# Performance work log

Measured on AMD Instinct MI355X. Metric: run time of the kernel, lower is better.

The kernel has to match this reference:

```python
import jax, jax.numpy as jnp
import numpy as np

EPS = 1e-5

def binary_activation(x):
    # ReActNet piecewise-polynomial STE: forward = sign(x), grad follows poly
    m1 = (x < -1).astype(x.dtype)
    m2 = (x < 0).astype(x.dtype)
    m3 = (x < 1).astype(x.dtype)
    out1 = -1.0 * m1 + (x * x + 2.0 * x) * (1.0 - m1)
    out2 = out1 * m2 + (-x * x + 2.0 * x) * (1.0 - m2)
    out3 = out2 * m3 + 1.0 * (1.0 - m3)
    return jax.lax.stop_gradient(jnp.sign(x) - out3) + out3

def binary_conv(x, w, stride, padding):
    # per-output-channel scaled sign weights with clamp STE
    scale = jnp.mean(jnp.abs(w), axis=(1, 2, 3), keepdims=True)
    clipped = jnp.clip(w, -1.0, 1.0)
    bw = jax.lax.stop_gradient(scale * jnp.sign(w) - clipped) + clipped
    return jax.lax.conv_general_dilated(
        x, bw, window_strides=(stride, stride),
        padding=[(padding, padding), (padding, padding)],
        dimension_numbers=('NCHW', 'OIHW', 'NCHW'))

def batch_norm(x, g, b):
    mu = jnp.mean(x, axis=(0, 2, 3), keepdims=True)
    var = jnp.mean((x - mu) ** 2, axis=(0, 2, 3), keepdims=True)
    xn = (x - mu) * jax.lax.rsqrt(var + EPS)
    return xn * g[None, :, None, None] + b[None, :, None, None]

def prelu(x, a):
    a = a[None, :, None, None]
    return jnp.where(x >= 0, x, a * x)

def setup_inputs() -> dict:
    key = jax.random.key(0)
    ks = jax.random.split(key, 12)
    N, C, H, W = 32, 256, 56, 56
    d = {
        'x': jax.random.normal(ks[0], (N, C, H, W), jnp.float32),
        'b11': jax.random.normal(ks[1], (1, C, 1, 1), jnp.float32) * 0.1,
        'b12': jax.random.normal(ks[2], (1, C, 1, 1), jnp.float32) * 0.1,
        'b13': jax.random.normal(ks[3], (1, C, 1, 1), jnp.float32) * 0.1,
        'b21': jax.random.normal(ks[4], (1, C, 1, 1), jnp.float32) * 0.1,
        'b22': jax.random.normal(ks[5], (1, C, 1, 1), jnp.float32) * 0.1,
        'b23': jax.random.normal(ks[6], (1, C, 1, 1), jnp.float32) * 0.1,
        'w3x3': jax.random.normal(ks[7], (C, C, 3, 3), jnp.float32) * 0.05,
        'wpw': jax.random.normal(ks[8], (C, C, 1, 1), jnp.float32) * 0.05,
        'g1': jnp.ones((C,), jnp.float32),
        'be1': jnp.zeros((C,), jnp.float32),
        'g2': jnp.ones((C,), jnp.float32),
        'be2': jnp.zeros((C,), jnp.float32),
        'p1': jnp.full((C,), 0.25, jnp.float32),
        'p2': jnp.full((C,), 0.25, jnp.float32),
    }
    return d

def reference(x, b11, b12, b13, b21, b22, b23, w3x3, wpw, g1, be1, g2, be2, p1, p2):
    # stride=1, inplanes == planes branch
    out1 = binary_activation(x + b11)
    out1 = binary_conv(out1, w3x3, stride=1, padding=1)
    out1 = batch_norm(out1, g1, be1)
    out1 = x + out1
    out1 = prelu(out1 + b12, p1) + b13
    out2 = binary_activation(out1 + b21)
    out2 = binary_conv(out2, wpw, stride=1, padding=0)
    out2 = batch_norm(out2, g2, be2)
    out2 = out2 + out1
    out2 = prelu(out2 + b22, p2) + b23
    return out2
```

## Files before the change

kernel.cpp:

```cpp
#include <hip/hip_runtime.h>

typedef __attribute__((ext_vector_type(4))) float  f32x4;
typedef __attribute__((ext_vector_type(4))) short  s16x4;
typedef __attribute__((ext_vector_type(4))) int    i32x4;

#define MFMAI8(a, b, c) __builtin_amdgcn_mfma_i32_16x16x64_i8((a), (b), (c), 0, 0, 0)

__device__ __forceinline__ void gload_lds16(const void* g, void* l) {
  __builtin_amdgcn_global_load_lds((const __attribute__((address_space(1))) void*)g,
                                   (__attribute__((address_space(3))) void*)l, 16, 0, 0);
}

__device__ __forceinline__ char sgn8(float v) {
  return v > 0.f ? (char)1 : (v < 0.f ? (char)-1 : (char)0);
}

__global__ __launch_bounds__(256) void prep_w(const float* __restrict__ w3,
                                              const float* __restrict__ wpw,
                                              char* __restrict__ w1s,
                                              char* __restrict__ w2s,
                                              float* __restrict__ scale1,
                                              float* __restrict__ scale2) {
  const int o = blockIdx.x;
  const int t = threadIdx.x;
  float s = 0.f;
  if (blockIdx.y == 0) {
    for (int u = t; u < 2304; u += 256) {
      int i = u / 9, tap = u % 9;
      float v = w3[(size_t)(o * 256 + i) * 9 + tap];
      s += fabsf(v);
      w1s[(size_t)(tap * 256 + o) * 256 + i] = sgn8(v);
    }
  } else {
    float v = wpw[o * 256 + t];
    s = fabsf(v);
    w2s[o * 256 + t] = sgn8(v);
  }
  for (int m = 1; m < 64; m <<= 1) s += __shfl_xor(s, m);
  __shared__ float red[4];
  if ((t & 63) == 0) red[t >> 6] = s;
  __syncthreads();
  if (t == 0) {
    float tot = red[0] + red[1] + red[2] + red[3];
    if (blockIdx.y == 0) scale1[o] = tot / 2304.f;
    else                 scale2[o] = tot / 256.f;
  }
}

__global__ __launch_bounds__(256) void sign_nhwc(const float* __restrict__ x,
                                                 const float* __restrict__ b11,
                                                 char* __restrict__ out) {
  __shared__ unsigned short l[56 * 128];
  __shared__ float cB[256];
  const int h = blockIdx.x, n = blockIdx.y, t = threadIdx.x;
  cB[t] = b11[t];
  __syncthreads();
  const int wv = t & 15, cg = t >> 4;
  if (wv < 14) {
    const int w0 = wv * 4;
    const int swz = (wv & 7) << 3;
#pragma unroll 4
    for (int it = 0; it < 8; ++it) {
      int cp = it * 16 + cg;
      int c0 = cp * 2;
      size_t i0 = (size_t)(n * 256 + c0) * 3136 + h * 56 + w0;
      f32x4 x0 = *(const f32x4*)(x + i0);
      f32x4 x1 = *(const f32x4*)(x + i0 + 3136);
      float bb0 = cB[c0], bb1 = cB[c0 + 1];
      int cs = cp ^ swz;
#pragma unroll
      for (int j = 0; j < 4; ++j) {
        unsigned short pk = (unsigned char)sgn8(x0[j] + bb0) |
                            ((unsigned short)(unsigned char)sgn8(x1[j] + bb1) << 8);
        l[(w0 + j) * 128 + cs] = pk;
      }
    }
  }
  __syncthreads();
  char* op = out + ((size_t)(n * 56 + h) * 56) * 256;
  for (int u = t; u < 56 * 16; u += 256) {
    int w2 = u >> 4, cp = u & 15;
    *(i32x4*)(op + w2 * 256 + cp * 16) =
        *(const i32x4*)&l[w2 * 128 + ((cp * 8) ^ (((w2 >> 2) & 7) << 3))];
  }
}

__global__ __launch_bounds__(256, 2) void conv3x3(const char* __restrict__ sIn,
                                                  const char* __restrict__ wSgn,
                                                  short* __restrict__ raw,
                                                  long long* __restrict__ S,
                                                  long long* __restrict__ SS) {
  __shared__ char lin[2][10 * 58 * 64];

  int bid = (blockIdx.x & 7) * 112 + (blockIdx.x >> 3);
  const int ot = bid & 3;
  const int g  = bid >> 2;
  const int ht = g % 7, n = g / 7;
  const int h0 = ht * 8, oc0 = ot * 64;

  const int t = threadIdx.x;
  const int lane = t & 63, wv = t >> 6;
  const int cl = lane & 15, kk = lane >> 4;

  if (t < 160) {
    int bi = t / 80, r = t % 80;
    int rr = r >> 3, q = r & 7;
    int col = (q >> 2) ? 57 : 0;
    *(i32x4*)&lin[bi][(rr * 58 + col) * 64 + (q & 3) * 16] = (i32x4){0, 0, 0, 0};
  }
  __syncthreads();

  const int pw = t >> 2, sl = t & 3;
  const int srcslot = sl ^ (((1 + pw) >> 1) & 3);

#define STAGE_3x3(icc, bi)                                                          \
  {                                                                                 \
    if (t < 224) {                                                                  \
      _Pragma("unroll")                                                             \
      for (int rr = 0; rr < 10; ++rr) {                                             \
        int h = h0 - 1 + rr;                                                        \
        char* dst = &lin[bi][(rr * 58 + 1 + pw) * 64 + sl * 16];                    \
        if (h >= 0 && h < 56) {                                                     \
          const char* src = sIn +                                                   \
              ((size_t)((n * 56 + h) * 56 + pw) * 256 + (icc) * 64 + srcslot * 16); \
          gload_lds16(src, dst);                                                    \
        } else {                                                                    \
          *(i32x4*)dst = (i32x4){0, 0, 0, 0};                                       \
        }                                                                           \
      }                                                                             \
    }                                                                               \
  }

  const char* wbase = wSgn + ((size_t)(oc0 + cl) << 8) + kk * 16;
#define WLOAD(dst, tap, icc)                                                        \
  {                                                                                 \
    _Pragma("unroll")                                                               \
    for (int m_ = 0; m_ < 4; ++m_)                                                  \
      dst[m_] = *(const i32x4*)(wbase + (size_t)(tap) * 65536 + m_ * 4096 + (icc) * 64); \
  }

  int r0[7], c0[7];
#pragma unroll
  for (int nf = 0; nf < 7; ++nf) {
    int p = wv * 112 + nf * 16 + cl;
    r0[nf] = p / 56;
    c0[nf] = p % 56;
  }

  i32x4 acc[4][7];
#pragma unroll
  for (int m = 0; m < 4; ++m)
#pragma unroll
    for (int nf = 0; nf < 7; ++nf) acc[m][nf] = (i32x4){0, 0, 0, 0};

  STAGE_3x3(0, 0);
  __syncthreads();

  i32x4 wA[4], wB[4];
  for (int icc = 0; icc < 4; ++icc) {
    const int cur = icc & 1;
    WLOAD(wA, 0, icc);
    WLOAD(wB, 1, icc);
    if (icc < 3) STAGE_3x3(icc + 1, cur ^ 1);

#pragma unroll
    for (int tap = 0; tap < 9; ++tap) {
      i32x4 w0 = wA[0], w1 = wA[1], w2 = wA[2], w3 = wA[3];
      wA[0] = wB[0]; wA[1] = wB[1]; wA[2] = wB[2]; wA[3] = wB[3];
      if (tap < 7) WLOAD(wB, tap + 2, icc);
      const int kh = tap / 3, kw = tap % 3;
#pragma unroll
      for (int nf = 0; nf < 7; ++nf) {
        int col = c0[nf] + kw;
        int addr = ((r0[nf] + kh) * 58 + col) * 64 + ((kk ^ ((col >> 1) & 3)) << 4);
        i32x4 b = *(const i32x4*)(&lin[cur][addr]);
        acc[0][nf] = MFMAI8(w0, b, acc[0][nf]);
        acc[1][nf] = MFMAI8(w1, b, acc[1][nf]);
        acc[2][nf] = MFMAI8(w2, b, acc[2][nf]);
        acc[3][nf] = MFMAI8(w3, b, acc[3][nf]);
      }
    }
    __syncthreads();
  }

  unsigned short* tb = (unsigned short*)&lin[0][0];
  const size_t ocbase = (size_t)n * 256 + oc0;
#pragma unroll
  for (int m = 0; m < 4; ++m) {
    int sm[4] = {0, 0, 0, 0};
    unsigned sq[4] = {0, 0, 0, 0};
#pragma unroll
    for (int nf = 0; nf < 7; ++nf) {
      i32x4 v = acc[m][nf];
#pragma unroll
      for (int r2 = 0; r2 < 4; ++r2) {
        sm[r2] += v[r2];
        sq[r2] += (unsigned)(v[r2] * v[r2]);
      }
    }
#pragma unroll
    for (int r2 = 0; r2 < 4; ++r2) {
      int aa = sm[r2];
      unsigned qq = sq[r2];
      aa += __shfl_xor(aa, 1); qq += __shfl_xor(qq, 1);
      aa += __shfl_xor(aa, 2); qq += __shfl_xor(qq, 2);
      aa += __shfl_xor(aa, 4); qq += __shfl_xor(qq, 4);
      aa += __shfl_xor(aa, 8); qq += __shfl_xor(qq, 8);
      if (cl == 0) {
        int oc = oc0 + m * 16 + kk * 4 + r2;
        atomicAdd((unsigned long long*)&S[oc], (unsigned long long)(long long)aa);
        atomicAdd((unsigned long long*)&SS[oc], (unsigned long long)qq);
      }
    }
    __syncthreads();
#pragma unroll
    for (int nf = 0; nf < 7; ++nf) {
      i32x4 v = acc[m][nf];
      int px = wv * 112 + nf * 16 + cl;
#pragma unroll
      for (int r2 = 0; r2 < 4; ++r2)
        tb[(kk * 4 + r2) * 472 + px] = (unsigned short)(short)v[r2];
    }
    __syncthreads();
    for (int u = t; u < 896; u += 256) {
      int qc = u >> 6, r = u & 63, ocl = r >> 2, c3 = r & 3;
      int c8 = qc * 4 + c3;
      *(i32x4*)(raw + (ocbase + m * 16 + ocl) * 3136 + h0 * 56 + c8 * 8) =
          *(const i32x4*)&tb[ocl * 472 + c8 * 8];
    }
  }
}

__global__ __launch_bounds__(256, 2) void conv1x1(const char* __restrict__ sIn,
                                                  const char* __restrict__ wSgn,
                                                  short* __restrict__ raw,
                                                  long long* __restrict__ S,
                                                  long long* __restrict__ SS) {
  __shared__ char lin[112 * 256];

  const int b = blockIdx.x;
  const int n = b / 28;
  const int hw0 = (b % 28) * 112;
  const size_t px0 = (size_t)n * 3136 + hw0;
  const int t = threadIdx.x, lane = t & 63, wv = t >> 6;
  const int cl = lane & 15, kk = lane >> 4;

#pragma unroll
  for (int i = 0; i < 7; ++i) {
    int u = i * 256 + t;
    int px = u >> 4, s = u & 15;
    const char* src = sIn + (px0 + px) * 256 + ((s ^ (px & 7)) * 16);
    gload_lds16(src, lin + u * 16);
  }

  i32x4 acc[4][7];
#pragma unroll
  for (int m = 0; m < 4; ++m)
#pragma unroll
    for (int nf = 0; nf < 7; ++nf) acc[m][nf] = (i32x4){0, 0, 0, 0};

  __syncthreads();

#pragma unroll
  for (int icc = 0; icc < 4; ++icc) {
    i32x4 bfr[7];
#pragma unroll
    for (int nf = 0; nf < 7; ++nf) {
      int px = nf * 16 + cl;
      int srd = (icc * 4 + kk) ^ (px & 7);
      bfr[nf] = *(const i32x4*)(lin + px * 256 + srd * 16);
    }
#pragma unroll
    for (int m = 0; m < 4; ++m) {
      i32x4 a = *(const i32x4*)(wSgn +
          (((size_t)(wv * 64 + m * 16 + cl)) << 8) + icc * 64 + kk * 16);
#pragma unroll
      for (int nf = 0; nf < 7; ++nf) acc[m][nf] = MFMAI8(a, bfr[nf], acc[m][nf]);
    }
  }

  __syncthreads();
  unsigned short* tb = (unsigned short*)lin;
#pragma unroll
  for (int m = 0; m < 4; ++m) {
    int sm[4] = {0, 0, 0, 0};
    unsigned sq[4] = {0, 0, 0, 0};
#pragma unroll
    for (int nf = 0; nf < 7; ++nf) {
      i32x4 v = acc[m][nf];
#pragma unroll
      for (int r2 = 0; r2 < 4; ++r2) {
        sm[r2] += v[r2];
        sq[r2] += (unsigned)(v[r2] * v[r2]);
      }
    }
#pragma unroll
    for (int r2 = 0; r2 < 4; ++r2) {
      int aa = sm[r2];
      unsigned qq = sq[r2];
      aa += __shfl_xor(aa, 1); qq += __shfl_xor(qq, 1);
      aa += __shfl_xor(aa, 2); qq += __shfl_xor(qq, 2);
      aa += __shfl_xor(aa, 4); qq += __shfl_xor(qq, 4);
      aa += __shfl_xor(aa, 8); qq += __shfl_xor(qq, 8);
      if (cl == 0) {
        int oc = wv * 64 + m * 16 + kk * 4 + r2;
        atomicAdd((unsigned long long*)&S[oc], (unsigned long long)(long long)aa);
        atomicAdd((unsigned long long*)&SS[oc], (unsigned long long)qq);
      }
    }
    __syncthreads();
#pragma unroll
    for (int nf = 0; nf < 7; ++nf) {
      i32x4 v = acc[m][nf];
      int px = nf * 16 + cl;
#pragma unroll
      for (int r2 = 0; r2 < 4; ++r2)
        tb[(wv * 16 + kk * 4 + r2) * 120 + px] = (unsigned short)(short)v[r2];
    }
    __syncthreads();
#pragma unroll
    for (int i = 0; i < 4; ++i) {
      int u = i * 256 + t;
      int ocg = u >> 4, c8 = u & 15;
      if (c8 < 14) {
        int oc = (ocg >> 4) * 64 + m * 16 + (ocg & 15);
        *(i32x4*)(raw + ((size_t)n * 256 + oc) * 3136 + hw0 + c8 * 8) =
            *(const i32x4*)&tb[ocg * 120 + c8 * 8];
      }
    }
  }
}

__global__ void bn_coef(const long long* __restrict__ S, const long long* __restrict__ SS,
                        const float* __restrict__ scale, const float* __restrict__ g,
                        const float* __restrict__ be, const float* __restrict__ bext,
                        float* __restrict__ A, float* __restrict__ B) {
  int o = threadIdx.x;
  const double invN = 1.0 / 100352.0;
  double mu_r  = (double)S[o] * invN;
  double var_r = (double)SS[o] * invN - mu_r * mu_r;
  double sc    = (double)scale[o];
  double rstd  = 1.0 / sqrt(sc * sc * var_r + 1e-5);
  double a     = (double)g[o] * rstd * sc;
  A[o] = (float)a;
  B[o] = (float)((double)be[o] - a * mu_r + (double)bext[o]);
}

__global__ __launch_bounds__(256) void mid_fuse(const short* __restrict__ raw,
                                                const float* __restrict__ x,
                                                const float* __restrict__ A1,
                                                const float* __restrict__ B1,
                                                const float* __restrict__ p1,
                                                const float* __restrict__ b13,
                                                const float* __restrict__ b21,
                                                float* __restrict__ t1,
                                                char* __restrict__ s2) {
  __shared__ unsigned short l[56 * 128];
  __shared__ float cA[256], cB[256], cP[256], cD[256], cE[256];
  const int h = blockIdx.x, n = blockIdx.y, t = threadIdx.x;
  cA[t] = A1[t]; cB[t] = B1[t]; cP[t] = p1[t]; cD[t] = b13[t]; cE[t] = b21[t];
  __syncthreads();
  const int wv = t & 15, cg = t >> 4;
  if (wv < 14) {
    const int w0 = wv * 4;
    const int swz = (wv & 7) << 3;
#pragma unroll 2
    for (int it = 0; it < 8; ++it) {
      int cp = it * 16 + cg;
      int c0 = cp * 2;
      size_t i0 = (size_t)(n * 256 + c0) * 3136 + h * 56 + w0;
      f32x4 x0 = *(const f32x4*)(x + i0);
      f32x4 x1 = *(const f32x4*)(x + i0 + 3136);
      s16x4 r0 = *(const s16x4*)(raw + i0);
      s16x4 r1 = *(const s16x4*)(raw + i0 + 3136);
      float a0 = cA[c0], b0 = cB[c0], p0 = cP[c0], d0 = cD[c0], e0 = cE[c0];
      float a1 = cA[c0+1], b1 = cB[c0+1], p1v = cP[c0+1], d1 = cD[c0+1], e1 = cE[c0+1];
      f32x4 o0, o1;
      int cs = cp ^ swz;
#pragma unroll
      for (int j = 0; j < 4; ++j) {
        float u0 = x0[j] + a0 * (float)r0[j] + b0;
        u0 = (u0 >= 0.f ? u0 : p0 * u0) + d0;
        o0[j] = u0;
        float u1 = x1[j] + a1 * (float)r1[j] + b1;
        u1 = (u1 >= 0.f ? u1 : p1v * u1) + d1;
        o1[j] = u1;
        unsigned short pk = (unsigned char)sgn8(u0 + e0) |
                            ((unsigned short)(unsigned char)sgn8(u1 + e1) << 8);
        l[(w0 + j) * 128 + cs] = pk;
      }
      *(f32x4*)(t1 + i0) = o0;
      *(f32x4*)(t1 + i0 + 3136) = o1;
    }
  }
  __syncthreads();
  char* op = s2 + ((size_t)(n * 56 + h) * 56) * 256;
  for (int u = t; u < 56 * 16; u += 256) {
    int w2 = u >> 4, cp = u & 15;
    *(i32x4*)(op + w2 * 256 + cp * 16) =
        *(const i32x4*)&l[w2 * 128 + ((cp * 8) ^ (((w2 >> 2) & 7) << 3))];
  }
}

__global__ __launch_bounds__(256) void final_fuse(const short* __restrict__ raw,
                                                  const float* __restrict__ A2,
                                                  const float* __restrict__ B2,
                                                  const float* __restrict__ p2,
                                                  const float* __restrict__ b23,
                                                  float* out) {
  const int c = blockIdx.x & 255;
  const size_t base = (size_t)blockIdx.x * 3136;
  const float a = A2[c], b = B2[c], p = p2[c], d = b23[c];
  for (int i = threadIdx.x; i < 784; i += 256) {
    s16x4 r  = *(const s16x4*)(raw + base + (size_t)i * 4);
    f32x4 tt = *(const f32x4*)(out + base + (size_t)i * 4);
    f32x4 o;
#pragma unroll
    for (int j = 0; j < 4; ++j) {
      float v = a * (float)r[j] + b + tt[j];
      o[j] = (v >= 0.f ? v : p * v) + d;
    }
    *(f32x4*)(out + base + (size_t)i * 4) = o;
  }
}

extern "C" void kernel_launch(void* const* d_in, const int* in_sizes, int n_in,
                              void* d_out, int out_size, void* d_ws, size_t ws_size,
                              hipStream_t stream) {
  const float* x   = (const float*)d_in[0];
  const float* b11 = (const float*)d_in[1];
  const float* b12 = (const float*)d_in[2];
  const float* b13 = (const float*)d_in[3];
  const float* b21 = (const float*)d_in[4];
  const float* b22 = (const float*)d_in[5];
  const float* b23 = (const float*)d_in[6];
  const float* w3  = (const float*)d_in[7];
  const float* wpw = (const float*)d_in[8];
  const float* g1  = (const float*)d_in[9];
  const float* be1 = (const float*)d_in[10];
  const float* g2  = (const float*)d_in[11];
  const float* be2 = (const float*)d_in[12];
  const float* p1  = (const float*)d_in[13];
  const float* p2  = (const float*)d_in[14];

  char* ws = (char*)d_ws;
  short*      raw    = (short*)(ws);
  char*       sgn    = (char*)(ws + 51380224);
  char*       w1s    = (char*)(ws + 77070336);
  char*       w2s    = (char*)(ws + 77660160);
  float*      scale1 = (float*)(ws + 77725696);
  float*      scale2 = (float*)(ws + 77726720);
  long long*  S1     = (long long*)(ws + 77727744);
  long long*  SS1    = (long long*)(ws + 77729792);
  long long*  S2     = (long long*)(ws + 77731840);
  long long*  SS2    = (long long*)(ws + 77733888);
  float*      A1     = (float*)(ws + 77735936);
  float*      B1     = (float*)(ws + 77736960);
  float*      A2     = (float*)(ws + 77737984);
  float*      B2     = (float*)(ws + 77739008);
  float*      t1     = (float*)d_out;

  hipMemsetAsync(ws + 77727744, 0, 8192, stream);

  prep_w<<<dim3(256, 2), 256, 0, stream>>>(w3, wpw, w1s, w2s, scale1, scale2);
  sign_nhwc<<<dim3(56, 32), 256, 0, stream>>>(x, b11, sgn);
  conv3x3<<<dim3(896), 256, 0, stream>>>(sgn, w1s, raw, S1, SS1);
  bn_coef<<<1, 256, 0, stream>>>(S1, SS1, scale1, g1, be1, b12, A1, B1);
  mid_fuse<<<dim3(56, 32), 256, 0, stream>>>(raw, x, A1, B1, p1, b13, b21, t1, sgn);
  conv1x1<<<dim3(896), 256, 0, stream>>>(sgn, w2s, raw, S2, SS2);
  bn_coef<<<1, 256, 0, stream>>>(S2, SS2, scale2, g2, be2, b22, A2, B2);
  final_fuse<<<dim3(8192), 256, 0, stream>>>(raw, A2, B2, p2, b23, (float*)d_out);
}
```

Before: 435.2 us.

## Retile conv3x3 to full-channel two-row tiles with single-shot input staging

The 3x3 binary conv block tile changes from 8 output rows by 64 output channels to 2 output rows by all 256 output channels. Each wave now owns 64 output channels. The whole 4-row, 256-input-channel halo is staged into LDS once with an XOR swizzle, and the double-buffered per-chunk staging is removed. The K loop is flattened into 36 steps with ping-pong weight registers. The aim is to remove repeated input staging and barriers and to reuse the input tile across all output channels. In exchange, halo re-reads grow (4 rows loaded for every 2 output) and weight global loads increase per block.

```diff
diff --git a/kernel.cpp b/kernel.cpp
--- a/kernel.cpp
+++ b/kernel.cpp
@@ -90,59 +90,35 @@
                                                   short* __restrict__ raw,
                                                   long long* __restrict__ S,
                                                   long long* __restrict__ SS) {
-  __shared__ char lin[2][10 * 58 * 64];
-
-  int bid = (blockIdx.x & 7) * 112 + (blockIdx.x >> 3);
-  const int ot = bid & 3;
-  const int g  = bid >> 2;
-  const int ht = g % 7, n = g / 7;
-  const int h0 = ht * 8, oc0 = ot * 64;
+  __shared__ char lin[4 * 58 * 256];
+
+  int g = (blockIdx.x & 7) * 112 + (blockIdx.x >> 3);
+  const int ht = g % 28, n = g / 28;
+  const int h0 = ht * 2;
 
   const int t = threadIdx.x;
   const int lane = t & 63, wv = t >> 6;
   const int cl = lane & 15, kk = lane >> 4;
 
-  if (t < 160) {
-    int bi = t / 80, r = t % 80;
-    int rr = r >> 3, q = r & 7;
-    int col = (q >> 2) ? 57 : 0;
-    *(i32x4*)&lin[bi][(rr * 58 + col) * 64 + (q & 3) * 16] = (i32x4){0, 0, 0, 0};
-  }
-  __syncthreads();
-
-  const int pw = t >> 2, sl = t & 3;
-  const int srcslot = sl ^ (((1 + pw) >> 1) & 3);
-
-#define STAGE_3x3(icc, bi)                                                          \
-  {                                                                                 \
-    if (t < 224) {                                                                  \
-      _Pragma("unroll")                                                             \
-      for (int rr = 0; rr < 10; ++rr) {                                             \
-        int h = h0 - 1 + rr;                                                        \
-        char* dst = &lin[bi][(rr * 58 + 1 + pw) * 64 + sl * 16];                    \
-        if (h >= 0 && h < 56) {                                                     \
-          const char* src = sIn +                                                   \
-              ((size_t)((n * 56 + h) * 56 + pw) * 256 + (icc) * 64 + srcslot * 16); \
-          gload_lds16(src, dst);                                                    \
-        } else {                                                                    \
-          *(i32x4*)dst = (i32x4){0, 0, 0, 0};                                       \
-        }                                                                           \
-      }                                                                             \
-    }                                                                               \
-  }
-
-  const char* wbase = wSgn + ((size_t)(oc0 + cl) << 8) + kk * 16;
-#define WLOAD(dst, tap, icc)                                                        \
-  {                                                                                 \
-    _Pragma("unroll")                                                               \
-    for (int m_ = 0; m_ < 4; ++m_)                                                  \
-      dst[m_] = *(const i32x4*)(wbase + (size_t)(tap) * 65536 + m_ * 4096 + (icc) * 64); \
+#pragma unroll
+  for (int i = 0; i < 15; ++i) {
+    int u = i * 256 + t;
+    if (u < 3712) {
+      int row = u / 928, rem = u % 928;
+      int col = rem >> 4, sl = rem & 15;
+      int h = h0 - 1 + row;
+      int hc = min(max(h, 0), 55);
+      int cc = min(max(col, 1), 56);
+      const char* src = sIn + ((size_t)((n * 56 + hc) * 56 + (cc - 1)) << 8) +
+                        ((sl ^ (col & 7)) << 4);
+      gload_lds16(src, lin + u * 16);
+    }
   }
 
   int r0[7], c0[7];
 #pragma unroll
   for (int nf = 0; nf < 7; ++nf) {
-    int p = wv * 112 + nf * 16 + cl;
+    int p = nf * 16 + cl;
     r0[nf] = p / 56;
     c0[nf] = p % 56;
   }
@@ -153,38 +129,58 @@
 #pragma unroll
     for (int nf = 0; nf < 7; ++nf) acc[m][nf] = (i32x4){0, 0, 0, 0};
 
-  STAGE_3x3(0, 0);
-  __syncthreads();
+  const char* wbase = wSgn + (((size_t)(wv * 64 + cl)) << 8) + kk * 16;
+#define WL(dst, kt_)                                                             \
+  {                                                                              \
+    const int icc_ = (kt_) / 9, tap_ = (kt_) % 9;                                \
+    _Pragma("unroll")                                                            \
+    for (int m_ = 0; m_ < 4; ++m_)                                               \
+      dst[m_] = *(const i32x4*)(wbase + tap_ * 65536 + m_ * 4096 + icc_ * 64);   \
+  }
 
   i32x4 wA[4], wB[4];
-  for (int icc = 0; icc < 4; ++icc) {
-    const int cur = icc & 1;
-    WLOAD(wA, 0, icc);
-    WLOAD(wB, 1, icc);
-    if (icc < 3) STAGE_3x3(icc + 1, cur ^ 1);
-
-#pragma unroll
-    for (int tap = 0; tap < 9; ++tap) {
-      i32x4 w0 = wA[0], w1 = wA[1], w2 = wA[2], w3 = wA[3];
-      wA[0] = wB[0]; wA[1] = wB[1]; wA[2] = wB[2]; wA[3] = wB[3];
-      if (tap < 7) WLOAD(wB, tap + 2, icc);
-      const int kh = tap / 3, kw = tap % 3;
-#pragma unroll
-      for (int nf = 0; nf < 7; ++nf) {
-        int col = c0[nf] + kw;
-        int addr = ((r0[nf] + kh) * 58 + col) * 64 + ((kk ^ ((col >> 1) & 3)) << 4);
-        i32x4 b = *(const i32x4*)(&lin[cur][addr]);
-        acc[0][nf] = MFMAI8(w0, b, acc[0][nf]);
-        acc[1][nf] = MFMAI8(w1, b, acc[1][nf]);
-        acc[2][nf] = MFMAI8(w2, b, acc[2][nf]);
-        acc[3][nf] = MFMAI8(w3, b, acc[3][nf]);
-      }
-    }
-    __syncthreads();
-  }
-
-  unsigned short* tb = (unsigned short*)&lin[0][0];
-  const size_t ocbase = (size_t)n * 256 + oc0;
+  WL(wA, 0);
+
+  __syncthreads();
+
+  if (t < 128) {
+    int row = t >> 5, cs = (t >> 4) & 1, sl = t & 15;
+    int col = cs ? 57 : 0;
+    *(i32x4*)(lin + (row * 58 + col) * 256 + sl * 16) = (i32x4){0, 0, 0, 0};
+  }
+  if (h0 == 0) {
+    for (int u = t; u < 928; u += 256)
+      *(i32x4*)(lin + u * 16) = (i32x4){0, 0, 0, 0};
+  }
+  if (h0 == 54) {
+    for (int u = t; u < 928; u += 256)
+      *(i32x4*)(lin + (3 * 928 + u) * 16) = (i32x4){0, 0, 0, 0};
+  }
+  __syncthreads();
+
+#pragma unroll
+  for (int kt = 0; kt < 36; ++kt) {
+    const int icc = kt / 9, tap = kt % 9;
+    const int kh = tap / 3, kw = tap % 3;
+    if (kt < 35) {
+      if (kt & 1) { WL(wA, kt + 1); } else { WL(wB, kt + 1); }
+    }
+#pragma unroll
+    for (int nf = 0; nf < 7; ++nf) {
+      int col = c0[nf] + kw;
+      int addr = ((r0[nf] + kh) * 58 + col) * 256 +
+                 (((icc * 4 + kk) ^ (col & 7)) << 4);
+      i32x4 b = *(const i32x4*)(lin + addr);
+#pragma unroll
+      for (int m = 0; m < 4; ++m) {
+        if (kt & 1) acc[m][nf] = MFMAI8(wB[m], b, acc[m][nf]);
+        else        acc[m][nf] = MFMAI8(wA[m], b, acc[m][nf]);
+      }
+    }
+  }
+
+  __syncthreads();
+  unsigned short* tb = (unsigned short*)lin;
 #pragma unroll
   for (int m = 0; m < 4; ++m) {
     int sm[4] = {0, 0, 0, 0};
@@ -207,7 +203,7 @@
       aa += __shfl_xor(aa, 4); qq += __shfl_xor(qq, 4);
       aa += __shfl_xor(aa, 8); qq += __shfl_xor(qq, 8);
       if (cl == 0) {
-        int oc = oc0 + m * 16 + kk * 4 + r2;
+        int oc = wv * 64 + m * 16 + kk * 4 + r2;
         atomicAdd((unsigned long long*)&S[oc], (unsigned long long)(long long)aa);
         atomicAdd((unsigned long long*)&SS[oc], (unsigned long long)qq);
       }
@@ -216,17 +212,21 @@
 #pragma unroll
     for (int nf = 0; nf < 7; ++nf) {
       i32x4 v = acc[m][nf];
-      int px = wv * 112 + nf * 16 + cl;
+      int px = nf * 16 + cl;
 #pragma unroll
       for (int r2 = 0; r2 < 4; ++r2)
-        tb[(kk * 4 + r2) * 472 + px] = (unsigned short)(short)v[r2];
+        tb[(wv * 16 + kk * 4 + r2) * 120 + px] = (unsigned short)(short)v[r2];
     }
     __syncthreads();
-    for (int u = t; u < 896; u += 256) {
-      int qc = u >> 6, r = u & 63, ocl = r >> 2, c3 = r & 3;
-      int c8 = qc * 4 + c3;
-      *(i32x4*)(raw + (ocbase + m * 16 + ocl) * 3136 + h0 * 56 + c8 * 8) =
-          *(const i32x4*)&tb[ocl * 472 + c8 * 8];
+#pragma unroll
+    for (int i = 0; i < 4; ++i) {
+      int u = i * 256 + t;
+      int ocg = u >> 4, c8 = u & 15;
+      if (c8 < 14) {
+        int oc = (ocg >> 4) * 64 + m * 16 + (ocg & 15);
+        *(i32x4*)(raw + ((size_t)n * 256 + oc) * 3136 + h0 * 56 + c8 * 8) =
+            *(const i32x4*)&tb[ocg * 120 + c8 * 8];
+      }
     }
   }
 }
```

Result: no change. 428.4 us (-1.6%).

## Stage 3x3 weights through LDS with depth-two async pipeline; pre-pack 1x1 weights

Applied to the files above, without the earlier changes.

The 3x3 conv now stages both the activation tile and the sign weights into LDS via async global-to-LDS loads. It double-buffers two input-channel chunks ahead, using explicit vmcnt waits and raw barriers, and zeroes the halo after the loads land instead of branching per row. The LDS budget roughly doubles, so launch bounds drop to one block per CU. The 1x1 conv weights are repacked in prep_w into MFMA fragment order and preloaded into registers up front, replacing strided per-iteration global loads. The risks are lower occupancy, more registers, and correctness depending on the hand-counted vmcnt threshold.

```diff
diff --git a/kernel.cpp b/kernel.cpp
--- a/kernel.cpp
+++ b/kernel.cpp
@@ -15,10 +15,15 @@
   return v > 0.f ? (char)1 : (v < 0.f ? (char)-1 : (char)0);
 }
 
+__device__ __forceinline__ void bar() {
+  __builtin_amdgcn_s_barrier();
+  __builtin_amdgcn_sched_barrier(0);
+}
+
 __global__ __launch_bounds__(256) void prep_w(const float* __restrict__ w3,
                                               const float* __restrict__ wpw,
                                               char* __restrict__ w1s,
-                                              char* __restrict__ w2s,
+                                              char* __restrict__ w2p,
                                               float* __restrict__ scale1,
                                               float* __restrict__ scale2) {
   const int o = blockIdx.x;
@@ -32,9 +37,11 @@
       w1s[(size_t)(tap * 256 + o) * 256 + i] = sgn8(v);
     }
   } else {
+    const int oct = o >> 6, mo = (o >> 4) & 3, cl = o & 15;
     float v = wpw[o * 256 + t];
     s = fabsf(v);
-    w2s[o * 256 + t] = sgn8(v);
+    size_t frag = (size_t)((t >> 6) * 4 + oct) * 4 + mo;
+    w2p[frag * 1024 + ((t >> 4) & 3) * 256 + cl * 16 + (t & 15)] = sgn8(v);
   }
   for (int m = 1; m < 64; m <<= 1) s += __shfl_xor(s, m);
   __shared__ float red[4];
@@ -85,58 +92,44 @@
   }
 }
 
-__global__ __launch_bounds__(256, 2) void conv3x3(const char* __restrict__ sIn,
+__global__ __launch_bounds__(256, 1) void conv3x3(const char* __restrict__ sIn,
                                                   const char* __restrict__ wSgn,
                                                   short* __restrict__ raw,
                                                   long long* __restrict__ S,
                                                   long long* __restrict__ SS) {
-  __shared__ char lin[2][10 * 58 * 64];
-
-  int bid = (blockIdx.x & 7) * 112 + (blockIdx.x >> 3);
-  const int ot = bid & 3;
-  const int g  = bid >> 2;
-  const int ht = g % 7, n = g / 7;
+  __shared__ char lin[2][10 * 64 * 64];
+  __shared__ char lw[2][9 * 64 * 64];
+
+  int g = (blockIdx.x & 7) * 112 + (blockIdx.x >> 3);
+  const int ot = g & 3;
+  const int gg = g >> 2;
+  const int ht = gg % 7, n = gg / 7;
   const int h0 = ht * 8, oc0 = ot * 64;
 
   const int t = threadIdx.x;
   const int lane = t & 63, wv = t >> 6;
   const int cl = lane & 15, kk = lane >> 4;
 
-  if (t < 160) {
-    int bi = t / 80, r = t % 80;
-    int rr = r >> 3, q = r & 7;
-    int col = (q >> 2) ? 57 : 0;
-    *(i32x4*)&lin[bi][(rr * 58 + col) * 64 + (q & 3) * 16] = (i32x4){0, 0, 0, 0};
-  }
-  __syncthreads();
-
-  const int pw = t >> 2, sl = t & 3;
-  const int srcslot = sl ^ (((1 + pw) >> 1) & 3);
-
-#define STAGE_3x3(icc, bi)                                                          \
-  {                                                                                 \
-    if (t < 224) {                                                                  \
-      _Pragma("unroll")                                                             \
-      for (int rr = 0; rr < 10; ++rr) {                                             \
-        int h = h0 - 1 + rr;                                                        \
-        char* dst = &lin[bi][(rr * 58 + 1 + pw) * 64 + sl * 16];                    \
-        if (h >= 0 && h < 56) {                                                     \
-          const char* src = sIn +                                                   \
-              ((size_t)((n * 56 + h) * 56 + pw) * 256 + (icc) * 64 + srcslot * 16); \
-          gload_lds16(src, dst);                                                    \
-        } else {                                                                    \
-          *(i32x4*)dst = (i32x4){0, 0, 0, 0};                                       \
-        }                                                                           \
-      }                                                                             \
-    }                                                                               \
-  }
-
-  const char* wbase = wSgn + ((size_t)(oc0 + cl) << 8) + kk * 16;
-#define WLOAD(dst, tap, icc)                                                        \
-  {                                                                                 \
-    _Pragma("unroll")                                                               \
-    for (int m_ = 0; m_ < 4; ++m_)                                                  \
-      dst[m_] = *(const i32x4*)(wbase + (size_t)(tap) * 65536 + m_ * 4096 + (icc) * 64); \
+#define STAGE(icc, bi)                                                          \
+  {                                                                             \
+    _Pragma("unroll")                                                           \
+    for (int i_ = 0; i_ < 10; ++i_) {                                           \
+      int u = i_ * 256 + t;                                                     \
+      int row = u >> 8, col = (u >> 2) & 63, sl = u & 3;                        \
+      int hc = min(max(h0 - 1 + row, 0), 55);                                   \
+      int wc = min(max(col, 1), 56) - 1;                                        \
+      const char* src = sIn + ((size_t)((n * 56 + hc) * 56 + wc) << 8) +        \
+                        (icc) * 64 + ((sl ^ ((col >> 1) & 3)) << 4);            \
+      gload_lds16(src, &lin[bi][u * 16]);                                       \
+    }                                                                           \
+    _Pragma("unroll")                                                           \
+    for (int i_ = 0; i_ < 9; ++i_) {                                            \
+      int u = i_ * 256 + t;                                                     \
+      int tap = u >> 8, oc_e = (u >> 2) & 63, sl = u & 3;                       \
+      const char* src = wSgn + ((size_t)(tap * 256 + oc0 + oc_e) << 8) +        \
+                        (icc) * 64 + ((sl ^ ((u >> 3) & 3)) << 4);              \
+      gload_lds16(src, &lw[bi][u * 16]);                                        \
+    }                                                                           \
   }
 
   int r0[7], c0[7];
@@ -153,34 +146,46 @@
 #pragma unroll
     for (int nf = 0; nf < 7; ++nf) acc[m][nf] = (i32x4){0, 0, 0, 0};
 
-  STAGE_3x3(0, 0);
-  __syncthreads();
-
-  i32x4 wA[4], wB[4];
+  STAGE(0, 0);
+  STAGE(1, 1);
+
   for (int icc = 0; icc < 4; ++icc) {
     const int cur = icc & 1;
-    WLOAD(wA, 0, icc);
-    WLOAD(wB, 1, icc);
-    if (icc < 3) STAGE_3x3(icc + 1, cur ^ 1);
+    if (icc < 3) { asm volatile("s_waitcnt vmcnt(19)" ::: "memory"); }
+    else         { asm volatile("s_waitcnt vmcnt(0)"  ::: "memory"); }
+    __builtin_amdgcn_sched_barrier(0);
+    bar();
+
+    if (t < 80) {
+      int row = t >> 3, q = t & 7;
+      int col = (q >> 2) ? 57 : 0;
+      *(i32x4*)&lin[cur][(row * 64 + col) * 64 + (q & 3) * 16] = (i32x4){0, 0, 0, 0};
+    }
+    if (ht == 0) *(i32x4*)&lin[cur][t * 16] = (i32x4){0, 0, 0, 0};
+    if (ht == 6) *(i32x4*)&lin[cur][(9 * 256 + t) * 16] = (i32x4){0, 0, 0, 0};
+    asm volatile("s_waitcnt lgkmcnt(0)" ::: "memory");
+    __builtin_amdgcn_sched_barrier(0);
+    bar();
 
 #pragma unroll
     for (int tap = 0; tap < 9; ++tap) {
-      i32x4 w0 = wA[0], w1 = wA[1], w2 = wA[2], w3 = wA[3];
-      wA[0] = wB[0]; wA[1] = wB[1]; wA[2] = wB[2]; wA[3] = wB[3];
-      if (tap < 7) WLOAD(wB, tap + 2, icc);
       const int kh = tap / 3, kw = tap % 3;
+      i32x4 a[4];
+#pragma unroll
+      for (int m = 0; m < 4; ++m)
+        a[m] = *(const i32x4*)&lw[cur][(tap * 64 + m * 16 + cl) * 64 +
+                                       ((kk ^ ((cl >> 1) & 3)) << 4)];
 #pragma unroll
       for (int nf = 0; nf < 7; ++nf) {
         int col = c0[nf] + kw;
-        int addr = ((r0[nf] + kh) * 58 + col) * 64 + ((kk ^ ((col >> 1) & 3)) << 4);
-        i32x4 b = *(const i32x4*)(&lin[cur][addr]);
-        acc[0][nf] = MFMAI8(w0, b, acc[0][nf]);
-        acc[1][nf] = MFMAI8(w1, b, acc[1][nf]);
-        acc[2][nf] = MFMAI8(w2, b, acc[2][nf]);
-        acc[3][nf] = MFMAI8(w3, b, acc[3][nf]);
-      }
-    }
-    __syncthreads();
+        int addr = ((r0[nf] + kh) * 64 + col) * 64 + ((kk ^ ((col >> 1) & 3)) << 4);
+        i32x4 b = *(const i32x4*)&lin[cur][addr];
+#pragma unroll
+        for (int m = 0; m < 4; ++m) acc[m][nf] = MFMAI8(a[m], b, acc[m][nf]);
+      }
+    }
+    bar();
+    if (icc < 2) STAGE(icc + 2, cur);
   }
 
   unsigned short* tb = (unsigned short*)&lin[0][0];
@@ -232,7 +237,7 @@
 }
 
 __global__ __launch_bounds__(256, 2) void conv1x1(const char* __restrict__ sIn,
-                                                  const char* __restrict__ wSgn,
+                                                  const char* __restrict__ w2p,
                                                   short* __restrict__ raw,
                                                   long long* __restrict__ S,
                                                   long long* __restrict__ SS) {
@@ -253,6 +258,14 @@
     gload_lds16(src, lin + u * 16);
   }
 
+  i32x4 wreg[4][4];
+#pragma unroll
+  for (int icc = 0; icc < 4; ++icc)
+#pragma unroll
+    for (int m = 0; m < 4; ++m)
+      wreg[icc][m] = *(const i32x4*)(w2p +
+          ((size_t)((icc * 4 + wv) * 4 + m)) * 1024 + lane * 16);
+
   i32x4 acc[4][7];
 #pragma unroll
   for (int m = 0; m < 4; ++m)
@@ -271,12 +284,10 @@
       bfr[nf] = *(const i32x4*)(lin + px * 256 + srd * 16);
     }
 #pragma unroll
-    for (int m = 0; m < 4; ++m) {
-      i32x4 a = *(const i32x4*)(wSgn +
-          (((size_t)(wv * 64 + m * 16 + cl)) << 8) + icc * 64 + kk * 16);
-#pragma unroll
-      for (int nf = 0; nf < 7; ++nf) acc[m][nf] = MFMAI8(a, bfr[nf], acc[m][nf]);
-    }
+    for (int m = 0; m < 4; ++m)
+#pragma unroll
+      for (int nf = 0; nf < 7; ++nf)
+        acc[m][nf] = MFMAI8(wreg[icc][m], bfr[nf], acc[m][nf]);
   }
 
   __syncthreads();
@@ -447,7 +458,7 @@
   short*      raw    = (short*)(ws);
   char*       sgn    = (char*)(ws + 51380224);
   char*       w1s    = (char*)(ws + 77070336);
-  char*       w2s    = (char*)(ws + 77660160);
+  char*       w2p    = (char*)(ws + 77660160);
   float*      scale1 = (float*)(ws + 77725696);
   float*      scale2 = (float*)(ws + 77726720);
   long long*  S1     = (long long*)(ws + 77727744);
@@ -462,12 +473,12 @@
 
   hipMemsetAsync(ws + 77727744, 0, 8192, stream);
 
-  prep_w<<<dim3(256, 2), 256, 0, stream>>>(w3, wpw, w1s, w2s, scale1, scale2);
+  prep_w<<<dim3(256, 2), 256, 0, stream>>>(w3, wpw, w1s, w2p, scale1, scale2);
   sign_nhwc<<<dim3(56, 32), 256, 0, stream>>>(x, b11, sgn);
   conv3x3<<<dim3(896), 256, 0, stream>>>(sgn, w1s, raw, S1, SS1);
   bn_coef<<<1, 256, 0, stream>>>(S1, SS1, scale1, g1, be1, b12, A1, B1);
   mid_fuse<<<dim3(56, 32), 256, 0, stream>>>(raw, x, A1, B1, p1, b13, b21, t1, sgn);
-  conv1x1<<<dim3(896), 256, 0, stream>>>(sgn, w2s, raw, S2, SS2);
+  conv1x1<<<dim3(896), 256, 0, stream>>>(sgn, w2p, raw, S2, SS2);
   bn_coef<<<1, 256, 0, stream>>>(S2, SS2, scale2, g2, be2, b22, A2, B2);
   final_fuse<<<dim3(8192), 256, 0, stream>>>(raw, A2, B2, p2, b23, (float*)d_out);
 }
```

After: 420.7 us. 1.03x faster.
